# Performance work log

Measured on AMD Instinct MI355X. Metric: run time of the kernel, lower is better.

## Reference

```python
import jax, jax.numpy as jnp
import numpy as np
import math

D_MODEL = 1024
NUM_HEADS = 16
D_HEAD = D_MODEL // NUM_HEADS          # 64
N_FREQ = D_HEAD // 2 + 1               # 33 rfft bins
COMPRESSION_RATIO = 0.5


def setup_inputs() -> dict:
    key = jax.random.key(0)
    k_x, k_qkv, k_out, k_b, k_m = jax.random.split(key, 5)
    B, S = 2, 2048
    x = jax.random.normal(k_x, (B, S, D_MODEL), dtype=jnp.float32)
    # Linear weights stored as [in, out] (torch Linear uses [out, in]; math identical).
    w_qkv = jax.random.normal(k_qkv, (D_MODEL, 3 * D_MODEL), dtype=jnp.float32) / math.sqrt(D_MODEL)
    w_out = jax.random.normal(k_out, (D_MODEL, D_MODEL), dtype=jnp.float32) / math.sqrt(D_MODEL)
    b_out = jax.random.normal(k_b, (D_MODEL,), dtype=jnp.float32) * 0.01
    # Learned per-frequency-bin mask logits of AdaptiveFrequencyMask(d_state=d_head).
    # Initialized around logit(compression_ratio) with small noise.
    init_logit = math.log(COMPRESSION_RATIO / (1.0 - COMPRESSION_RATIO))
    mask_logits = init_logit + 0.1 * jax.random.normal(k_m, (N_FREQ,), dtype=jnp.float32)
    return {"x": x, "w_qkv": w_qkv, "w_out": w_out, "b_out": b_out, "mask_logits": mask_logits}


def _spectral_filter(t, mask):
    # rfft over d_head dim, apply learned soft mask, inverse rfft.  t: [B,H,S,dh]
    tf = jnp.fft.rfft(t, axis=-1)          # [B,H,S,N_FREQ] complex
    tf = tf * mask                          # broadcast real mask over bins
    return jnp.fft.irfft(tf, n=t.shape[-1], axis=-1).astype(t.dtype)


def reference(x, w_qkv, w_out, b_out, mask_logits):
    B, S, D = x.shape
    H, dh = NUM_HEADS, D_HEAD
    qkv = x @ w_qkv                                         # [B,S,3D]
    q, k, v = jnp.split(qkv, 3, axis=-1)
    # [B,S,D] -> [B,H,S,dh]
    to_heads = lambda t: t.reshape(B, S, H, dh).transpose(0, 2, 1, 3)
    q, k, v = to_heads(q), to_heads(k), to_heads(v)
    mask = jax.nn.sigmoid(mask_logits)                      # [N_FREQ]
    q = _spectral_filter(q, mask)
    k = _spectral_filter(k, mask)
    scores = jnp.einsum('bhqd,bhkd->bhqk', q, k) / math.sqrt(dh)
    attn = jax.nn.softmax(scores, axis=-1)                  # dropout p=0 (eval)
    out = jnp.einsum('bhqk,bhkd->bhqd', attn, v)
    out = out.transpose(0, 2, 1, 3).reshape(B, S, D)
    return out @ w_out + b_out
```

## Files before the change

### kernel.cpp

```cpp
#include <hip/hip_runtime.h>

#define S_LEN 2048
#define NH    16
#define DH    64
#define DM    1024
#define NQKV  3072

typedef __attribute__((ext_vector_type(8))) __bf16 bf16x8;
typedef __attribute__((ext_vector_type(4))) float  f32x4;
typedef unsigned short ushort_t;

static __device__ __forceinline__ unsigned short bf16b(float f) {
  return __builtin_bit_cast(unsigned short, (__bf16)f);
}

static __device__ __forceinline__ float exp2v(float x) {
  return __builtin_amdgcn_exp2f(x);
}

static __device__ __forceinline__ bf16x8 pack8(float4 f0, float4 f1) {
  uint4 v;
  v.x = ((unsigned)bf16b(f0.y) << 16) | bf16b(f0.x);
  v.y = ((unsigned)bf16b(f0.w) << 16) | bf16b(f0.z);
  v.z = ((unsigned)bf16b(f1.y) << 16) | bf16b(f1.x);
  v.w = ((unsigned)bf16b(f1.w) << 16) | bf16b(f1.z);
  return __builtin_bit_cast(bf16x8, v);
}

static __device__ __forceinline__ void glds16(const void* g, void* l) {
  __builtin_amdgcn_global_load_lds((const __attribute__((address_space(1))) unsigned int*)g,
                                   (__attribute__((address_space(3))) unsigned int*)l, 16, 0, 0);
}

#define OFF_WT  65536ull
#define OFF_WOT 6356992ull
#define OFF_Q   8454144ull
#define OFF_K   16842752ull
#define OFF_V   25231360ull
#define OFF_AO  33619968ull

__global__ __launch_bounds__(256) void k_prep(const float* __restrict__ wqkv,
                                              const float* __restrict__ wout,
                                              const float* __restrict__ x,
                                              const float* __restrict__ logits,
                                              unsigned short* __restrict__ Wt,
                                              unsigned short* __restrict__ Wot,
                                              unsigned short* __restrict__ xb) {
  __shared__ __align__(16) char sbuf[16640];
  int bid = blockIdx.x;
  int t = threadIdx.x;

  if (bid < 256) {
    float* msk = (float*)sbuf;
    float* Kd  = (float*)(sbuf + 144);
    ushort_t (*Fb)[72] = (ushort_t(*)[72])(sbuf + 416);
    if (t < 33) msk[t] = 1.0f / (1.0f + __expf(-logits[t]));
    __syncthreads();
    if (t < 64) {
      float acc = msk[0];
      #pragma unroll
      for (int f = 1; f < 32; ++f) {
        int r = (f * t) & 63;
        acc += 2.0f * msk[f] * __cosf((float)r * (6.28318530717958647692f / 64.0f));
      }
      acc += msk[32] * ((t & 1) ? -1.0f : 1.0f);
      Kd[t] = acc * (1.0f / 64.0f);
    }
    __syncthreads();
    for (int idx = t; idx < 4096; idx += 256) {
      int j = idx >> 6, i = idx & 63;
      Fb[j][i] = bf16b(Kd[(j - i) & 63]);
    }
    __syncthreads();

    int lane = t & 63, w = t >> 6;
    int m16 = lane & 15, quad = lane >> 4;
    int kx = bid >> 5, yy = bid & 31;
    int which = yy >> 4, h = yy & 15;
    int base = which * 1024 + h * 64;

    bf16x8 af0 = *(const bf16x8*)(&Fb[w * 16 + m16][quad * 8]);
    bf16x8 af1 = *(const bf16x8*)(&Fb[w * 16 + m16][32 + quad * 8]);

    f32x4 acc[8] = {};
    #pragma unroll 2
    for (int n = 0; n < 8; ++n) {
      const float* Wg = wqkv + (size_t)(kx * 128 + n * 16 + m16) * NQKV + base + quad * 8;
      float4 a0 = *(const float4*)(Wg);
      float4 a1 = *(const float4*)(Wg + 4);
      float4 b0 = *(const float4*)(Wg + 32);
      float4 b1 = *(const float4*)(Wg + 36);
      acc[n] = __builtin_amdgcn_mfma_f32_16x16x32_bf16(af0, pack8(a0, a1), acc[n], 0, 0, 0);
      acc[n] = __builtin_amdgcn_mfma_f32_16x16x32_bf16(af1, pack8(b0, b1), acc[n], 0, 0, 0);
    }
    float sc = (which == 0) ? 0.18033688011112042f : 1.0f;
    #pragma unroll
    for (int n = 0; n < 8; ++n) {
      #pragma unroll
      for (int r = 0; r < 4; ++r) {
        int j = w * 16 + quad * 4 + r;
        Wt[(size_t)(base + j) * DM + kx * 128 + n * 16 + m16] = bf16b(acc[n][r] * sc);
      }
    }
  } else if (bid < 768) {
    float (*Ts)[65] = (float(*)[65])sbuf;
    int b1 = bid - 256;
    if (b1 < 256) {
      int kt = b1 & 15, nt = b1 >> 4;
      int cb = 2048 + nt * 64, kbase = kt * 64;
      #pragma unroll
      for (int p = 0; p < 16; ++p) {
        int kk = p * 4 + (t >> 6);
        Ts[kk][t & 63] = wqkv[(size_t)(kbase + kk) * NQKV + cb + (t & 63)];
      }
      __syncthreads();
      #pragma unroll
      for (int p = 0; p < 16; ++p) {
        int nn = p * 4 + (t >> 6);
        Wt[(size_t)(cb + nn) * DM + kbase + (t & 63)] = bf16b(Ts[t & 63][nn]);
      }
    } else {
      int b2 = b1 - 256;
      int kt = b2 & 15, nt = b2 >> 4;
      int cb = nt * 64, kbase = kt * 64;
      #pragma unroll
      for (int p = 0; p < 16; ++p) {
        int kk = p * 4 + (t >> 6);
        Ts[kk][t & 63] = wout[(size_t)(kbase + kk) * DM + cb + (t & 63)];
      }
      __syncthreads();
      #pragma unroll
      for (int p = 0; p < 16; ++p) {
        int nn = p * 4 + (t >> 6);
        Wot[(size_t)(cb + nn) * DM + kbase + (t & 63)] = bf16b(Ts[t & 63][nn]);
      }
    }
  } else {
    size_t i = ((size_t)(bid - 768) * 256 + t) * 8;
    const float4* xp = (const float4*)(x + i);
    float4 a = xp[0], b = xp[1];
    uint4 v;
    v.x = ((unsigned)bf16b(a.y) << 16) | bf16b(a.x);
    v.y = ((unsigned)bf16b(a.w) << 16) | bf16b(a.z);
    v.z = ((unsigned)bf16b(b.y) << 16) | bf16b(b.x);
    v.w = ((unsigned)bf16b(b.w) << 16) | bf16b(b.z);
    *(uint4*)(xb + i) = v;
  }
}

__device__ __forceinline__ void gemm_core_async(const unsigned short* __restrict__ A,
                                                const unsigned short* __restrict__ Bw,
                                                int bm, int bn, unsigned short* smem,
                                                f32x4 (&acc)[4][4]) {
  unsigned short* As = smem;
  unsigned short* Bs = smem + 8192;
  int t = threadIdx.x, lane = t & 63, w = t >> 6;
  int m16 = lane & 15, quad = lane >> 4;
  int wr = (w >> 1) * 64, wc = (w & 1) * 64;
  int lr = lane >> 3, lc = lane & 7;
  int gc = lc ^ lr;
  int xr = m16 & 7;
  const unsigned short* Agb = A  + (size_t)(bm * 128) * DM + gc * 8;
  const unsigned short* Bgb = Bw + (size_t)(bn * 128) * DM + gc * 8;

  for (int k0 = 0; k0 < DM; k0 += 64) {
    #pragma unroll
    for (int p = 0; p < 4; ++p) {
      int row = p * 32 + w * 8 + lr;
      glds16(Agb + (size_t)row * DM + k0, As + row * 64 + lc * 8);
      glds16(Bgb + (size_t)row * DM + k0, Bs + row * 64 + lc * 8);
    }
    __syncthreads();
    #pragma unroll
    for (int kk = 0; kk < 2; ++kk) {
      bf16x8 af[4], bfr[4];
      #pragma unroll
      for (int i = 0; i < 4; ++i)
        af[i] = *(const bf16x8*)(As + (wr + i * 16 + m16) * 64 + ((kk * 4 + quad) ^ xr) * 8);
      #pragma unroll
      for (int j = 0; j < 4; ++j)
        bfr[j] = *(const bf16x8*)(Bs + (wc + j * 16 + m16) * 64 + ((kk * 4 + quad) ^ xr) * 8);
      #pragma unroll
      for (int i = 0; i < 4; ++i)
        #pragma unroll
        for (int j = 0; j < 4; ++j)
          acc[i][j] = __builtin_amdgcn_mfma_f32_16x16x32_bf16(af[i], bfr[j], acc[i][j], 0, 0, 0);
    }
    __syncthreads();
  }
}

__global__ __launch_bounds__(256) void k_gemm_qkv(const unsigned short* __restrict__ xb,
                                                  const unsigned short* __restrict__ Bw,
                                                  unsigned short* __restrict__ Qb,
                                                  unsigned short* __restrict__ Kb,
                                                  unsigned short* __restrict__ Vt) {
  __shared__ __align__(16) unsigned short smem[18432];
  f32x4 acc[4][4] = {};
  int bn = blockIdx.x, bm = blockIdx.y;
  gemm_core_async(xb, Bw, bm, bn, smem, acc);

  int t = threadIdx.x, lane = t & 63, w = t >> 6;
  int m16 = lane & 15, quad = lane >> 4;
  int wr = (w >> 1) * 64, wc = (w & 1) * 64;
  int b = bm >> 4, srow = (bm & 15) * 128;
  int which = bn >> 3;
  ushort_t (*Tr)[130] = (ushort_t(*)[130])smem;
  if (which < 2) {
    #pragma unroll
    for (int i = 0; i < 4; ++i)
      #pragma unroll
      for (int j = 0; j < 4; ++j)
        #pragma unroll
        for (int r = 0; r < 4; ++r)
          Tr[wr + i * 16 + quad * 4 + r][wc + j * 16 + m16] = bf16b(acc[i][j][r]);
    __syncthreads();
    int row = t >> 1, half = t & 1;
    int cloc = bn * 128 + half * 64 - which * 1024;
    int h = cloc >> 6;
    unsigned short* dst = (which ? Kb : Qb) +
        ((size_t)(b * 16 + h) * 2048 + srow + row) * 64;
    #pragma unroll
    for (int p = 0; p < 8; ++p)
      *(uint4*)(dst + p * 8) = *(const uint4*)(&Tr[row][half * 64 + p * 8]);
  } else {
    #pragma unroll
    for (int i = 0; i < 4; ++i)
      #pragma unroll
      for (int j = 0; j < 4; ++j)
        #pragma unroll
        for (int r = 0; r < 4; ++r)
          Tr[wc + j * 16 + m16][wr + i * 16 + quad * 4 + r] = bf16b(acc[i][j][r]);
    __syncthreads();
    int dl = t >> 1, half = t & 1;
    int cloc = (bn - 16) * 128 + dl;
    int h = cloc >> 6, d = cloc & 63;
    unsigned short* dst = Vt + ((size_t)(b * 16 + h) * 64 + d) * 2048 + srow + half * 64;
    #pragma unroll
    for (int p = 0; p < 8; ++p)
      *(uint4*)(dst + p * 8) = *(const uint4*)(&Tr[dl][half * 64 + p * 8]);
  }
}

__global__ __launch_bounds__(512, 4) void k_attn(const unsigned short* __restrict__ Qb,
                                                 const unsigned short* __restrict__ Kb,
                                                 const unsigned short* __restrict__ Vt,
                                                 unsigned short* __restrict__ AO) {
  __shared__ __align__(16) unsigned short smem[25088];
  int t = threadIdx.x;
  int w = t >> 6, lane = t & 63;
  int m16 = lane & 15, quad = lane >> 4;
  int bid = blockIdx.x;
  int jj = bid >> 3;
  int bh = ((jj & 3) << 3) + (bid & 7);
  int qbase = (jj >> 2) * 128 + w * 16;

  const unsigned short* Qp = Qb + ((size_t)bh * S_LEN + qbase + m16) * DH + quad * 8;
  bf16x8 aq0 = *(const bf16x8*)(Qp);
  bf16x8 aq1 = *(const bf16x8*)(Qp + 32);
  const unsigned short* Kbase = Kb + (size_t)bh * S_LEN * DH;
  const unsigned short* Vbase = Vt + (size_t)bh * DH * S_LEN;

  unsigned short* Pw = smem + 16384 + w * 1088;
  int xr = m16 & 7;

  int trow = t >> 3;
  int tcol = t & 7;
  int gswz = tcol ^ (trow & 7);

  f32x4 o[4] = {};
  float l = 0.f;
  f32x4 zero = {0.f, 0.f, 0.f, 0.f};

  glds16(Kbase + (size_t)trow * 64 + gswz * 8,    smem + trow * 64 + tcol * 8);
  glds16(Vbase + (size_t)trow * S_LEN + gswz * 8, smem + 8192 + trow * 64 + tcol * 8);
  __syncthreads();

  #pragma unroll 1
  for (int kt = 0; kt < S_LEN / 64; ++kt) {
    int cur = kt & 1, nxt = cur ^ 1;
    if (kt + 1 < S_LEN / 64) {
      int kk = (kt + 1) * 64;
      glds16(Kbase + (size_t)(kk + trow) * 64 + gswz * 8,
             smem + nxt * 4096 + trow * 64 + tcol * 8);
      glds16(Vbase + (size_t)trow * S_LEN + kk + gswz * 8,
             smem + 8192 + nxt * 4096 + trow * 64 + tcol * 8);
    }
    unsigned short* Ksh = smem + cur * 4096;
    unsigned short* Vsh = smem + 8192 + cur * 4096;

    f32x4 st[4];
    #pragma unroll
    for (int g = 0; g < 4; ++g) {
      int rk = g * 16 + m16;
      bf16x8 kf0 = *(const bf16x8*)(Ksh + rk * 64 + ((quad ^ xr) * 8));
      bf16x8 kf1 = *(const bf16x8*)(Ksh + rk * 64 + (((4 + quad) ^ xr) * 8));
      st[g] = __builtin_amdgcn_mfma_f32_16x16x32_bf16(kf0, aq0, zero, 0, 0, 0);
      st[g] = __builtin_amdgcn_mfma_f32_16x16x32_bf16(kf1, aq1, st[g], 0, 0, 0);
    }
    #pragma unroll
    for (int g = 0; g < 4; ++g) {
      float p0 = exp2v(st[g][0]), p1 = exp2v(st[g][1]);
      float p2 = exp2v(st[g][2]), p3 = exp2v(st[g][3]);
      l += (p0 + p1) + (p2 + p3);
      uint2 pk;
      pk.x = ((unsigned)bf16b(p1) << 16) | bf16b(p0);
      pk.y = ((unsigned)bf16b(p3) << 16) | bf16b(p2);
      *(uint2*)(Pw + m16 * 68 + g * 16 + quad * 4) = pk;
    }
    #pragma unroll
    for (int c = 0; c < 2; ++c) {
      bf16x8 ap = *(const bf16x8*)(Pw + m16 * 68 + c * 32 + quad * 8);
      #pragma unroll
      for (int j = 0; j < 4; ++j) {
        int dv = j * 16 + m16;
        bf16x8 bv = *(const bf16x8*)(Vsh + dv * 64 + (((c * 4 + quad) ^ xr) * 8));
        o[j] = __builtin_amdgcn_mfma_f32_16x16x32_bf16(ap, bv, o[j], 0, 0, 0);
      }
    }
    __syncthreads();
  }

  l += __shfl_xor(l, 16); l += __shfl_xor(l, 32);
  float iv = 1.0f / l;
  int b = bh >> 4, h = bh & 15;
  #pragma unroll
  for (int r = 0; r < 4; ++r) {
    float v0 = __shfl(iv, quad * 4 + r);
    size_t row0 = (size_t)b * S_LEN + qbase + quad * 4 + r;
    unsigned short* d0 = AO + row0 * DM + h * DH + m16;
    #pragma unroll
    for (int j = 0; j < 4; ++j)
      d0[j * 16] = bf16b(o[j][r] * v0);
  }
}

__global__ __launch_bounds__(256) void k_gemm_out(const unsigned short* __restrict__ A,
                                                  const unsigned short* __restrict__ Bw,
                                                  const float* __restrict__ bias,
                                                  float* __restrict__ out) {
  __shared__ __align__(16) unsigned short smem[18432];
  f32x4 acc[4][4] = {};
  int bn = blockIdx.x, bm = blockIdx.y;
  gemm_core_async(A, Bw, bm, bn, smem, acc);

  int t = threadIdx.x, lane = t & 63, w = t >> 6;
  int m16 = lane & 15, quad = lane >> 4;
  int wr = (w >> 1) * 64, wc = (w & 1) * 64;
  #pragma unroll
  for (int i = 0; i < 4; ++i) {
    int grow = bm * 128 + wr + i * 16 + quad * 4;
    #pragma unroll
    for (int j = 0; j < 4; ++j) {
      int gc = bn * 128 + wc + j * 16 + m16;
      float bb = bias[gc];
      #pragma unroll
      for (int r = 0; r < 4; ++r)
        out[(size_t)(grow + r) * DM + gc] = acc[i][j][r] + bb;
    }
  }
}

extern "C" void kernel_launch(void* const* d_in, const int* in_sizes, int n_in,
                              void* d_out, int out_size, void* d_ws, size_t ws_size,
                              hipStream_t stream) {
  const float* x    = (const float*)d_in[0];
  const float* wqkv = (const float*)d_in[1];
  const float* wout = (const float*)d_in[2];
  const float* bout = (const float*)d_in[3];
  const float* mlog = (const float*)d_in[4];
  char* ws = (char*)d_ws;
  unsigned short* Wt  = (unsigned short*)(ws + OFF_WT);
  unsigned short* Wot = (unsigned short*)(ws + OFF_WOT);
  unsigned short* Qb  = (unsigned short*)(ws + OFF_Q);
  unsigned short* Kb  = (unsigned short*)(ws + OFF_K);
  unsigned short* Vt  = (unsigned short*)(ws + OFF_V);
  unsigned short* xb  = (unsigned short*)(ws + OFF_AO);
  unsigned short* AO  = (unsigned short*)(ws + OFF_AO);
  float* out = (float*)d_out;

  k_prep<<<dim3(2816), dim3(256), 0, stream>>>(wqkv, wout, x, mlog, Wt, Wot, xb);
  k_gemm_qkv<<<dim3(24, 32), dim3(256), 0, stream>>>(xb, Wt, Qb, Kb, Vt);
  k_attn<<<dim3(512), dim3(512), 0, stream>>>(Qb, Kb, Vt, AO);
  k_gemm_out<<<dim3(8, 32), dim3(256), 0, stream>>>(AO, Wot, bout, out);
}
```

Before: 219.6 us.

## Triple-buffer K/V tiles in attention with one barrier per iteration

The attention kernel moves from double to triple buffering of its K and V shared-memory tiles, prefetching two tiles ahead. A partial vmcnt wait plus a single barrier at the top of each iteration replaces the end-of-loop __syncthreads. The MFMA phases are also wrapped in s_setprio raises so waves doing matrix work get issue priority. This is meant to hide global-load latency and cut synchronisation cost, at the price of more LDS per block, which may lower occupancy.

```diff
diff --git a/kernel.cpp b/kernel.cpp
--- a/kernel.cpp
+++ b/kernel.cpp
@@ -246,7 +246,7 @@
                                                  const unsigned short* __restrict__ Kb,
                                                  const unsigned short* __restrict__ Vt,
                                                  unsigned short* __restrict__ AO) {
-  __shared__ __align__(16) unsigned short smem[25088];
+  __shared__ __align__(16) unsigned short smem[33280];
   int t = threadIdx.x;
   int w = t >> 6, lane = t & 63;
   int m16 = lane & 15, quad = lane >> 4;
@@ -261,35 +261,42 @@
   const unsigned short* Kbase = Kb + (size_t)bh * S_LEN * DH;
   const unsigned short* Vbase = Vt + (size_t)bh * DH * S_LEN;
 
-  unsigned short* Pw = smem + 16384 + w * 1088;
+  unsigned short* Pw = smem + 24576 + w * 1088;
   int xr = m16 & 7;
 
   int trow = t >> 3;
   int tcol = t & 7;
   int gswz = tcol ^ (trow & 7);
+  const unsigned short* Kg = Kbase + (size_t)trow * 64 + gswz * 8;
+  const unsigned short* Vg = Vbase + (size_t)trow * S_LEN + gswz * 8;
+  unsigned short* Kl = smem + trow * 64 + tcol * 8;
+  unsigned short* Vl = smem + 12288 + trow * 64 + tcol * 8;
 
   f32x4 o[4] = {};
   float l = 0.f;
   f32x4 zero = {0.f, 0.f, 0.f, 0.f};
 
-  glds16(Kbase + (size_t)trow * 64 + gswz * 8,    smem + trow * 64 + tcol * 8);
-  glds16(Vbase + (size_t)trow * S_LEN + gswz * 8, smem + 8192 + trow * 64 + tcol * 8);
-  __syncthreads();
-
+  glds16(Kg,        Kl);
+  glds16(Vg,        Vl);
+  glds16(Kg + 4096, Kl + 4096);
+  glds16(Vg + 64,   Vl + 4096);
+
+  int buf = 0, slot = 2;
   #pragma unroll 1
   for (int kt = 0; kt < S_LEN / 64; ++kt) {
-    int cur = kt & 1, nxt = cur ^ 1;
-    if (kt + 1 < S_LEN / 64) {
-      int kk = (kt + 1) * 64;
-      glds16(Kbase + (size_t)(kk + trow) * 64 + gswz * 8,
-             smem + nxt * 4096 + trow * 64 + tcol * 8);
-      glds16(Vbase + (size_t)trow * S_LEN + kk + gswz * 8,
-             smem + 8192 + nxt * 4096 + trow * 64 + tcol * 8);
-    }
-    unsigned short* Ksh = smem + cur * 4096;
-    unsigned short* Vsh = smem + 8192 + cur * 4096;
+    if (kt + 1 < S_LEN / 64) asm volatile("s_waitcnt vmcnt(2)" ::: "memory");
+    else                     asm volatile("s_waitcnt vmcnt(0)" ::: "memory");
+    __builtin_amdgcn_s_barrier();
+    __builtin_amdgcn_sched_barrier(0);
+    if (kt + 2 < S_LEN / 64) {
+      glds16(Kg + (size_t)(kt + 2) * 4096, Kl + slot * 4096);
+      glds16(Vg + (kt + 2) * 64,           Vl + slot * 4096);
+    }
+    unsigned short* Ksh = smem + buf * 4096;
+    unsigned short* Vsh = smem + 12288 + buf * 4096;
 
     f32x4 st[4];
+    __builtin_amdgcn_s_setprio(1);
     #pragma unroll
     for (int g = 0; g < 4; ++g) {
       int rk = g * 16 + m16;
@@ -298,6 +305,7 @@
       st[g] = __builtin_amdgcn_mfma_f32_16x16x32_bf16(kf0, aq0, zero, 0, 0, 0);
       st[g] = __builtin_amdgcn_mfma_f32_16x16x32_bf16(kf1, aq1, st[g], 0, 0, 0);
     }
+    __builtin_amdgcn_s_setprio(0);
     #pragma unroll
     for (int g = 0; g < 4; ++g) {
       float p0 = exp2v(st[g][0]), p1 = exp2v(st[g][1]);
@@ -308,6 +316,7 @@
       pk.y = ((unsigned)bf16b(p3) << 16) | bf16b(p2);
       *(uint2*)(Pw + m16 * 68 + g * 16 + quad * 4) = pk;
     }
+    __builtin_amdgcn_s_setprio(1);
     #pragma unroll
     for (int c = 0; c < 2; ++c) {
       bf16x8 ap = *(const bf16x8*)(Pw + m16 * 68 + c * 32 + quad * 8);
@@ -318,7 +327,9 @@
         o[j] = __builtin_amdgcn_mfma_f32_16x16x32_bf16(ap, bv, o[j], 0, 0, 0);
       }
     }
-    __syncthreads();
+    __builtin_amdgcn_s_setprio(0);
+    buf  = (buf  == 2) ? 0 : buf  + 1;
+    slot = (slot == 2) ? 0 : slot + 1;
   }
 
   l += __shfl_xor(l, 16); l += __shfl_xor(l, 32);
```

New measurement: 215.5 us. Within noise of the previous version (-1.9%).
